# Optimization experiments

Measured on AMD Instinct MI355X. Metric: run time of the kernel, lower is better.

Reference implementation:

```python
import jax, jax.numpy as jnp
import numpy as np

N, D_IN, D_OUT, E, K = 32768, 1024, 1024, 8, 2
LN_EPS = 1e-5


def setup_inputs() -> dict:
    key = jax.random.key(0)
    ks = jax.random.split(key, 7)
    x = jax.random.normal(ks[0], (N, D_IN), dtype=jnp.float32)
    # gate: Linear(D_IN, E) then Tanh
    Wg = jax.random.normal(ks[1], (D_IN, E), dtype=jnp.float32) * 0.02
    bg = jnp.zeros((E,), dtype=jnp.float32)
    # experts: stacked Linear(D_IN, D_OUT) weights, [E, D_IN, D_OUT]
    We = jax.random.normal(ks[2], (E, D_IN, D_OUT), dtype=jnp.float32) * 0.02
    be = jnp.zeros((E, D_OUT), dtype=jnp.float32)
    # per-expert LayerNorm params
    gamma = jnp.ones((E, D_OUT), dtype=jnp.float32)
    beta = jnp.zeros((E, D_OUT), dtype=jnp.float32)
    return {"x": x, "Wg": Wg, "bg": bg, "We": We, "be": be,
            "gamma": gamma, "beta": beta}


def reference(x, Wg, bg, We, be, gamma, beta):
    # gating: Linear + Tanh, then top-k over experts, softmax over the k gates
    gate_logits = jnp.tanh(x @ Wg + bg)                      # [N, E]
    top_g, top_i = jax.lax.top_k(gate_logits, K)             # [N, K], [N, K]
    gates = jax.nn.softmax(top_g, axis=-1)                   # [N, K]

    # all experts computed densely (faithful to original): Linear + GELU + LN
    h = jnp.einsum('ni,eio->neo', x, We) + be[None]          # [N, E, D_OUT]
    h = jax.nn.gelu(h, approximate=False)                    # torch nn.GELU (exact)
    mu = jnp.mean(h, axis=-1, keepdims=True)
    var = jnp.mean(jnp.square(h - mu), axis=-1, keepdims=True)
    h = (h - mu) * jax.lax.rsqrt(var + LN_EPS)
    h = h * gamma[None] + beta[None]                         # [N, E, D_OUT]

    # gather top-k expert outputs and combine with softmax gates
    sel = jnp.take_along_axis(h, top_i[:, :, None], axis=1)  # [N, K, D_OUT]
    return jnp.sum(sel * gates[:, :, None], axis=1)          # [N, D_OUT]
```

## Files before the change

### kernel.cpp

```cpp
#include <hip/hip_runtime.h>
#include <hip/hip_bf16.h>

#define N_TOK 32768
#define D_IN 1024
#define D_OUT 1024
#define NE 8

#define BM 128
#define BN 128
#define BK 64
#define PAD 72

#define GBLK 64
#define GCH 64
#define NCH (D_IN / GCH)
#define CNT_STRIDE 64

typedef __attribute__((ext_vector_type(8))) short short8;
typedef __attribute__((ext_vector_type(4))) float floatx4;

__device__ __forceinline__ unsigned short f2bf(float f) {
    union { float f; unsigned u; } v; v.f = f;
    unsigned r = v.u + 0x7fffu + ((v.u >> 16) & 1u);
    return (unsigned short)(r >> 16);
}
__device__ __forceinline__ float bf2f(unsigned short u) {
    union { unsigned u; float f; } v; v.u = ((unsigned)u) << 16;
    return v.f;
}

__global__ void zero_cnt(int* __restrict__ cnt) {
    int i = blockIdx.x * 256 + threadIdx.x;
    if (i < 16 * CNT_STRIDE) cnt[i] = 0;
}

__global__ __launch_bounds__(256) void transpose_we(
    const float* __restrict__ We, unsigned short* __restrict__ WeT)
{
    __shared__ unsigned short tile[64 * 65];
    int e = blockIdx.z;
    int i0 = blockIdx.x * 64, o0 = blockIdx.y * 64;
    const float* src = We + ((size_t)e * D_IN + i0) * D_OUT + o0;
#pragma unroll
    for (int it = 0; it < 16; ++it) {
        int idx = threadIdx.x + it * 256;
        int r = idx >> 6, c = idx & 63;
        tile[r * 65 + c] = f2bf(src[(size_t)r * D_OUT + c]);
    }
    __syncthreads();
    unsigned short* dst = WeT + ((size_t)e * D_OUT + o0) * D_IN + i0;
#pragma unroll
    for (int it = 0; it < 16; ++it) {
        int idx = threadIdx.x + it * 256;
        int r = idx >> 6, c = idx & 63;
        dst[(size_t)r * D_IN + c] = tile[c * 65 + r];
    }
}

__global__ __launch_bounds__(256) void gate_kernel(
    const float* __restrict__ x, const float* __restrict__ Wg,
    const float* __restrict__ bg,
    int* __restrict__ top_i, float* __restrict__ gates,
    int* __restrict__ cnt, int* __restrict__ lists,
    unsigned short* __restrict__ xb)
{
    __shared__ float xs[GBLK][GCH + 1];
    __shared__ float wgs[4][136];
    __shared__ int lcnt[16];
    __shared__ int lbase[16];
    __shared__ int ltoks[16][GBLK];

    int tid = threadIdx.x;
    if (tid < 16) lcnt[tid] = 0;

    int tok0 = blockIdx.x * GBLK;
    int lane = tid & 63, wave = tid >> 6;
    int t = lane >> 2, q = lane & 3;
    int row = wave * 16 + t;
    int token = tok0 + row;

    double acc[NE] = {};

#pragma unroll 1
    for (int c = 0; c < NCH; ++c) {
        int cb = c * GCH;
        __syncthreads();
        {
            int i = tid;
#pragma unroll
            for (int it = 0; it < 2; ++it, i += 256) {
                float v = Wg[(size_t)cb * NE + i];
                int d = i >> 3, e = i & 7;
                wgs[d >> 4][(d & 15) * 8 + e] = v;
            }
        }
#pragma unroll
        for (int it = 0; it < 4; ++it) {
            int idx = tid + it * 256;
            int r = idx >> 4, c4 = (idx & 15) * 4;
            const float4 v = *(const float4*)(x + (size_t)(tok0 + r) * D_IN + cb + c4);
            xs[r][c4 + 0] = v.x; xs[r][c4 + 1] = v.y;
            xs[r][c4 + 2] = v.z; xs[r][c4 + 3] = v.w;
            ushort4 pk;
            pk.x = f2bf(v.x); pk.y = f2bf(v.y); pk.z = f2bf(v.z); pk.w = f2bf(v.w);
            *(ushort4*)(xb + (size_t)(tok0 + r) * D_IN + cb + c4) = pk;
        }
        __syncthreads();
#pragma unroll
        for (int jj = 0; jj < 16; ++jj) {
            double xd = (double)xs[row][q * 16 + jj];
            const float* wr = &wgs[q][jj * 8];
#pragma unroll
            for (int e = 0; e < NE; ++e)
                acc[e] += xd * (double)wr[e];
        }
    }

#pragma unroll
    for (int off = 1; off <= 2; off <<= 1)
#pragma unroll
        for (int e = 0; e < NE; ++e)
            acc[e] += __shfl_xor(acc[e], off, 64);

    float lg[NE];
#pragma unroll
    for (int e = 0; e < NE; ++e) lg[e] = tanhf((float)(acc[e] + (double)bg[e]));
    int i0 = 0;
    for (int e = 1; e < NE; ++e) if (lg[e] > lg[i0]) i0 = e;
    int i1 = (i0 == 0) ? 1 : 0;
    for (int e = 0; e < NE; ++e) { if (e == i0) continue; if (lg[e] > lg[i1]) i1 = e; }
    float tt = expf(lg[i1] - lg[i0]);
    float g0 = 1.0f / (1.0f + tt);
    float g1 = tt * g0;

    if (q == 0) {
        top_i[token * 2 + 0] = i0; top_i[token * 2 + 1] = i1;
        gates[token * 2 + 0] = g0; gates[token * 2 + 1] = g1;
        int p0 = atomicAdd(&lcnt[i0], 1);
        ltoks[i0][p0] = token;
        int p1 = atomicAdd(&lcnt[NE + i1], 1);
        ltoks[NE + i1][p1] = token;
    }
    __syncthreads();
    if (tid < 16) lbase[tid] = atomicAdd(&cnt[tid * CNT_STRIDE], lcnt[tid]);
    __syncthreads();
    int g = tid >> 4, j = tid & 15;
    int n = lcnt[g];
    int* dst = lists + (size_t)g * N_TOK + lbase[g];
    for (int k = j; k < n; k += 16) dst[k] = ltoks[g][k];
}

template <bool USEBF>
__global__ __launch_bounds__(256) void gemm_slot(
    const float* __restrict__ x, const unsigned short* __restrict__ xb,
    const unsigned short* __restrict__ WeT,
    const float* __restrict__ be, const int* __restrict__ lists,
    const int* __restrict__ cnt, int slot, unsigned short* __restrict__ h)
{
    int e = blockIdx.z;
    int count = cnt[(slot * NE + e) * CNT_STRIDE];
    int m0 = blockIdx.y * BM;
    if (m0 >= count) return;
    int n0 = blockIdx.x * BN;
    const int* list = lists + (size_t)(slot * NE + e) * N_TOK;

    __shared__ int toks[BM];
    __shared__ unsigned short As[BM * PAD];
    __shared__ unsigned short Bs[BN * PAD];

    int tid = threadIdx.x;
    if (tid < BM) {
        int r = m0 + tid; if (r > count - 1) r = count - 1;
        toks[tid] = list[r];
    }
    __syncthreads();

    int lane = tid & 63, wave = tid >> 6;
    int wm = (wave & 1) * 64, wn = (wave >> 1) * 64;
    int q = lane & 15, quad = lane >> 4;

    floatx4 acc[4][4] = {};

    const unsigned short* Bglob = WeT + ((size_t)e * D_OUT + n0) * D_IN;

    for (int kb = 0; kb < D_IN; kb += BK) {
        if (USEBF) {
#pragma unroll
            for (int it = 0; it < 4; ++it) {
                int idx = tid + it * 256;
                int m = idx >> 3, kq = idx & 7;
                *(uint4*)&As[m * PAD + kq * 8] =
                    *(const uint4*)(xb + (size_t)toks[m] * D_IN + kb + kq * 8);
            }
        } else {
#pragma unroll
            for (int it = 0; it < 8; ++it) {
                int idx = tid + it * 256;
                int m = idx >> 4, kq = idx & 15;
                float4 v = *(const float4*)(x + (size_t)toks[m] * D_IN + kb + kq * 4);
                ushort4 pk;
                pk.x = f2bf(v.x); pk.y = f2bf(v.y); pk.z = f2bf(v.z); pk.w = f2bf(v.w);
                *(ushort4*)&As[m * PAD + kq * 4] = pk;
            }
        }
#pragma unroll
        for (int it = 0; it < 4; ++it) {
            int idx = tid + it * 256;
            int n = idx >> 3, kq = idx & 7;
            *(uint4*)&Bs[n * PAD + kq * 8] =
                *(const uint4*)(Bglob + (size_t)n * D_IN + kb + kq * 8);
        }
        __syncthreads();

#pragma unroll
        for (int ks = 0; ks < BK; ks += 32) {
            short8 af[4], bfr[4];
#pragma unroll
            for (int i = 0; i < 4; ++i)
                af[i] = *(const short8*)&As[(wm + i * 16 + q) * PAD + ks + quad * 8];
#pragma unroll
            for (int j = 0; j < 4; ++j)
                bfr[j] = *(const short8*)&Bs[(wn + j * 16 + q) * PAD + ks + quad * 8];
#pragma unroll
            for (int i = 0; i < 4; ++i)
#pragma unroll
                for (int j = 0; j < 4; ++j)
                    acc[i][j] = __builtin_amdgcn_mfma_f32_16x16x32_bf16(
                        af[i], bfr[j], acc[i][j], 0, 0, 0);
        }
        __syncthreads();
    }

#pragma unroll
    for (int i = 0; i < 4; ++i) {
#pragma unroll
        for (int r = 0; r < 4; ++r) {
            int m = wm + i * 16 + quad * 4 + r;
            if (m0 + m < count) {
                int tok = toks[m];
#pragma unroll
                for (int j = 0; j < 4; ++j) {
                    int n = n0 + wn + j * 16 + q;
                    float v = acc[i][j][r] + be[(size_t)e * D_OUT + n];
                    h[(size_t)tok * D_OUT + n] = f2bf(v);
                }
            }
        }
    }
}

__global__ __launch_bounds__(256) void ln_combine(
    const unsigned short* __restrict__ h, const float* __restrict__ gamma,
    const float* __restrict__ beta, const float* __restrict__ gates,
    const int* __restrict__ top_i, int slot, float* __restrict__ out)
{
    int wave = threadIdx.x >> 6, lane = threadIdx.x & 63;
    int token = blockIdx.x * 4 + wave;
    int e = top_i[token * 2 + slot];
    float gate = gates[token * 2 + slot];
    const unsigned short* hr = h + (size_t)token * D_OUT;

    float g[16], sum = 0.f, sumsq = 0.f;
#pragma unroll
    for (int jj = 0; jj < 4; ++jj) {
        int n = jj * 256 + lane * 4;
        uint2 pk = *(const uint2*)(hr + n);
        float v0 = bf2f((unsigned short)(pk.x & 0xffff));
        float v1 = bf2f((unsigned short)(pk.x >> 16));
        float v2 = bf2f((unsigned short)(pk.y & 0xffff));
        float v3 = bf2f((unsigned short)(pk.y >> 16));
        float g0 = 0.5f * v0 * (1.0f + erff(v0 * 0.70710678118654752f));
        float g1 = 0.5f * v1 * (1.0f + erff(v1 * 0.70710678118654752f));
        float g2 = 0.5f * v2 * (1.0f + erff(v2 * 0.70710678118654752f));
        float g3 = 0.5f * v3 * (1.0f + erff(v3 * 0.70710678118654752f));
        g[jj * 4 + 0] = g0; g[jj * 4 + 1] = g1; g[jj * 4 + 2] = g2; g[jj * 4 + 3] = g3;
        sum   += g0 + g1 + g2 + g3;
        sumsq += g0 * g0 + g1 * g1 + g2 * g2 + g3 * g3;
    }
#pragma unroll
    for (int off = 32; off; off >>= 1) {
        sum   += __shfl_xor(sum, off, 64);
        sumsq += __shfl_xor(sumsq, off, 64);
    }
    float mu  = sum * (1.0f / 1024.0f);
    float var = sumsq * (1.0f / 1024.0f) - mu * mu;
    float rs  = rsqrtf(var + 1e-5f);

    const float* gm = gamma + (size_t)e * D_OUT;
    const float* bt = beta  + (size_t)e * D_OUT;
    float* orow = out + (size_t)token * D_OUT;
#pragma unroll
    for (int jj = 0; jj < 4; ++jj) {
        int n = jj * 256 + lane * 4;
        float4 gm4 = *(const float4*)(gm + n);
        float4 bt4 = *(const float4*)(bt + n);
        float4 o;
        o.x = gate * ((g[jj * 4 + 0] - mu) * rs * gm4.x + bt4.x);
        o.y = gate * ((g[jj * 4 + 1] - mu) * rs * gm4.y + bt4.y);
        o.z = gate * ((g[jj * 4 + 2] - mu) * rs * gm4.z + bt4.z);
        o.w = gate * ((g[jj * 4 + 3] - mu) * rs * gm4.w + bt4.w);
        if (slot == 0) {
            *(float4*)(orow + n) = o;
        } else {
            float4 p = *(const float4*)(orow + n);
            p.x += o.x; p.y += o.y; p.z += o.z; p.w += o.w;
            *(float4*)(orow + n) = p;
        }
    }
}

extern "C" void kernel_launch(void* const* d_in, const int* in_sizes, int n_in,
                              void* d_out, int out_size, void* d_ws, size_t ws_size,
                              hipStream_t stream) {
    const float* x     = (const float*)d_in[0];
    const float* Wg    = (const float*)d_in[1];
    const float* bg    = (const float*)d_in[2];
    const float* We    = (const float*)d_in[3];
    const float* be    = (const float*)d_in[4];
    const float* gamma = (const float*)d_in[5];
    const float* beta  = (const float*)d_in[6];
    float* out = (float*)d_out;

    char* w = (char*)d_ws;
    size_t off = 0;
    int*   cnt   = (int*)(w + off);            off += (size_t)16 * CNT_STRIDE * 4;
    int*   top_i = (int*)(w + off);            off += (size_t)N_TOK * 2 * 4;
    float* gates = (float*)(w + off);          off += (size_t)N_TOK * 2 * 4;
    int*   lists = (int*)(w + off);            off += (size_t)16 * N_TOK * 4;
    unsigned short* WeT = (unsigned short*)(w + off); off += (size_t)NE * D_IN * D_OUT * 2;
    unsigned short* h   = (unsigned short*)(w + off); off += (size_t)N_TOK * D_OUT * 2;
    size_t xb_bytes = (size_t)N_TOK * D_IN * 2;
    bool use_bf = (off + xb_bytes) <= ws_size;
    unsigned short* xb = use_bf ? (unsigned short*)(w + off) : h;
    if (use_bf) off += xb_bytes;

    zero_cnt<<<(16 * CNT_STRIDE + 255) / 256, 256, 0, stream>>>(cnt);
    transpose_we<<<dim3(16, 16, NE), 256, 0, stream>>>(We, WeT);
    gate_kernel<<<N_TOK / GBLK, 256, 0, stream>>>(x, Wg, bg, top_i, gates, cnt, lists, xb);
    for (int s = 0; s < 2; ++s) {
        if (use_bf)
            gemm_slot<true><<<dim3(D_OUT / BN, N_TOK / BM, NE), 256, 0, stream>>>(
                x, xb, WeT, be, lists, cnt, s, h);
        else
            gemm_slot<false><<<dim3(D_OUT / BN, N_TOK / BM, NE), 256, 0, stream>>>(
                x, xb, WeT, be, lists, cnt, s, h);
        ln_combine<<<N_TOK / 4, 256, 0, stream>>>(h, gamma, beta, gates, top_i, s, out);
    }
}
```

Before: 644.4 us.

## Use direct global-to-LDS loads with XOR swizzle and fuse both slots

The bf16 GEMM now loads A and B tiles straight into LDS with global_load_lds, using an XOR-swizzled unpadded layout in place of the register-staged padded copy. When workspace allows, both top-k slots run in a single GEMM launch that writes two separate h buffers, and a new combine kernel normalises both expert outputs and writes the output once instead of doing a read-modify-write. The aim is to cut VGPR staging and load latency, drop kernel launches, and halve traffic on the output. It needs an extra N×D_OUT bf16 workspace buffer, and the swizzle and LDS-destination indexing must line up with the per-wave write pattern of the direct loads.

```diff
diff --git a/kernel.cpp b/kernel.cpp
--- a/kernel.cpp
+++ b/kernel.cpp
@@ -16,6 +16,9 @@
 #define NCH (D_IN / GCH)
 #define CNT_STRIDE 64
 
+#define AS1 __attribute__((address_space(1)))
+#define AS3 __attribute__((address_space(3)))
+
 typedef __attribute__((ext_vector_type(8))) short short8;
 typedef __attribute__((ext_vector_type(4))) float floatx4;
 
@@ -27,6 +30,11 @@
 __device__ __forceinline__ float bf2f(unsigned short u) {
     union { unsigned u; float f; } v; v.u = ((unsigned)u) << 16;
     return v.f;
+}
+
+__device__ __forceinline__ void gl_lds16(const void* g, void* l) {
+    __builtin_amdgcn_global_load_lds((const AS1 unsigned int*)g,
+                                     (AS3 unsigned int*)l, 16, 0, 0);
 }
 
 __global__ void zero_cnt(int* __restrict__ cnt) {
@@ -150,9 +158,113 @@
     for (int k = j; k < n; k += 16) dst[k] = ltoks[g][k];
 }
 
-template <bool USEBF>
-__global__ __launch_bounds__(256) void gemm_slot(
-    const float* __restrict__ x, const unsigned short* __restrict__ xb,
+__global__ __launch_bounds__(256) void gemm_slot2(
+    const unsigned short* __restrict__ xb,
+    const unsigned short* __restrict__ WeT,
+    const float* __restrict__ be, const int* __restrict__ lists,
+    const int* __restrict__ cnt, int zoff,
+    unsigned short* __restrict__ h0, unsigned short* __restrict__ h1)
+{
+    int z = blockIdx.z + zoff;
+    int slot = z >> 3, e = z & 7;
+    unsigned short* __restrict__ h = slot ? h1 : h0;
+    int count = cnt[z * CNT_STRIDE];
+    int m0 = blockIdx.y * BM;
+    if (m0 >= count) return;
+    int n0 = blockIdx.x * BN;
+    const int* list = lists + (size_t)z * N_TOK;
+
+    __shared__ int toks[BM];
+    __shared__ __align__(16) unsigned short As[BM * BK];
+    __shared__ __align__(16) unsigned short Bs[BN * BK];
+
+    int tid = threadIdx.x;
+    if (tid < BM) {
+        int r = m0 + tid; if (r > count - 1) r = count - 1;
+        toks[tid] = list[r];
+    }
+    __syncthreads();
+
+    int lane = tid & 63, wave = tid >> 6;
+    int wm = (wave & 1) * 64, wn = (wave >> 1) * 64;
+    int q = lane & 15, quad = lane >> 4;
+
+    const unsigned short* Bglob = WeT + ((size_t)e * D_OUT + n0) * D_IN;
+
+    const unsigned short* asrc[4];
+    const unsigned short* bsrc[4];
+    unsigned short* adst[4];
+    unsigned short* bdst[4];
+#pragma unroll
+    for (int it = 0; it < 4; ++it) {
+        int idx = tid + it * 256;
+        int m = idx >> 3, c = idx & 7;
+        int sc = c ^ (m & 7);
+        asrc[it] = xb + (size_t)toks[m] * D_IN + sc * 8;
+        bsrc[it] = Bglob + (size_t)m * D_IN + sc * 8;
+        unsigned short* base = (unsigned short*)0;
+        adst[it] = As + (size_t)(it * 256 + (tid & 192)) * 8;
+        bdst[it] = Bs + (size_t)(it * 256 + (tid & 192)) * 8;
+        (void)base;
+    }
+
+    floatx4 acc[4][4] = {};
+
+    for (int kb = 0; kb < D_IN; kb += BK) {
+#pragma unroll
+        for (int it = 0; it < 4; ++it)
+            gl_lds16(asrc[it] + kb, adst[it]);
+#pragma unroll
+        for (int it = 0; it < 4; ++it)
+            gl_lds16(bsrc[it] + kb, bdst[it]);
+        __syncthreads();
+
+#pragma unroll
+        for (int ks = 0; ks < BK; ks += 32) {
+            int cb = ks >> 3;
+            short8 af[4], bfr[4];
+#pragma unroll
+            for (int i = 0; i < 4; ++i) {
+                int row = wm + i * 16 + q;
+                int ch = (cb + quad) ^ (row & 7);
+                af[i] = *(const short8*)&As[row * BK + ch * 8];
+            }
+#pragma unroll
+            for (int j = 0; j < 4; ++j) {
+                int row = wn + j * 16 + q;
+                int ch = (cb + quad) ^ (row & 7);
+                bfr[j] = *(const short8*)&Bs[row * BK + ch * 8];
+            }
+#pragma unroll
+            for (int i = 0; i < 4; ++i)
+#pragma unroll
+                for (int j = 0; j < 4; ++j)
+                    acc[i][j] = __builtin_amdgcn_mfma_f32_16x16x32_bf16(
+                        af[i], bfr[j], acc[i][j], 0, 0, 0);
+        }
+        __syncthreads();
+    }
+
+#pragma unroll
+    for (int i = 0; i < 4; ++i) {
+#pragma unroll
+        for (int r = 0; r < 4; ++r) {
+            int m = wm + i * 16 + quad * 4 + r;
+            if (m0 + m < count) {
+                int tok = toks[m];
+#pragma unroll
+                for (int j = 0; j < 4; ++j) {
+                    int n = n0 + wn + j * 16 + q;
+                    float v = acc[i][j][r] + be[(size_t)e * D_OUT + n];
+                    h[(size_t)tok * D_OUT + n] = f2bf(v);
+                }
+            }
+        }
+    }
+}
+
+__global__ __launch_bounds__(256) void gemm_slot_f32(
+    const float* __restrict__ x,
     const unsigned short* __restrict__ WeT,
     const float* __restrict__ be, const int* __restrict__ lists,
     const int* __restrict__ cnt, int slot, unsigned short* __restrict__ h)
@@ -180,28 +292,17 @@
     int q = lane & 15, quad = lane >> 4;
 
     floatx4 acc[4][4] = {};
-
     const unsigned short* Bglob = WeT + ((size_t)e * D_OUT + n0) * D_IN;
 
     for (int kb = 0; kb < D_IN; kb += BK) {
-        if (USEBF) {
-#pragma unroll
-            for (int it = 0; it < 4; ++it) {
-                int idx = tid + it * 256;
-                int m = idx >> 3, kq = idx & 7;
-                *(uint4*)&As[m * PAD + kq * 8] =
-                    *(const uint4*)(xb + (size_t)toks[m] * D_IN + kb + kq * 8);
-            }
-        } else {
-#pragma unroll
-            for (int it = 0; it < 8; ++it) {
-                int idx = tid + it * 256;
-                int m = idx >> 4, kq = idx & 15;
-                float4 v = *(const float4*)(x + (size_t)toks[m] * D_IN + kb + kq * 4);
-                ushort4 pk;
-                pk.x = f2bf(v.x); pk.y = f2bf(v.y); pk.z = f2bf(v.z); pk.w = f2bf(v.w);
-                *(ushort4*)&As[m * PAD + kq * 4] = pk;
-            }
+#pragma unroll
+        for (int it = 0; it < 8; ++it) {
+            int idx = tid + it * 256;
+            int m = idx >> 4, kq = idx & 15;
+            float4 v = *(const float4*)(x + (size_t)toks[m] * D_IN + kb + kq * 4);
+            ushort4 pk;
+            pk.x = f2bf(v.x); pk.y = f2bf(v.y); pk.z = f2bf(v.z); pk.w = f2bf(v.w);
+            *(ushort4*)&As[m * PAD + kq * 4] = pk;
         }
 #pragma unroll
         for (int it = 0; it < 4; ++it) {
@@ -211,7 +312,6 @@
                 *(const uint4*)(Bglob + (size_t)n * D_IN + kb + kq * 8);
         }
         __syncthreads();
-
 #pragma unroll
         for (int ks = 0; ks < BK; ks += 32) {
             short8 af[4], bfr[4];
@@ -309,6 +409,76 @@
     }
 }
 
+__global__ __launch_bounds__(256) void ln_combine2(
+    const unsigned short* __restrict__ h0, const unsigned short* __restrict__ h1,
+    const float* __restrict__ gamma, const float* __restrict__ beta,
+    const float* __restrict__ gates, const int* __restrict__ top_i,
+    float* __restrict__ out)
+{
+    int wave = threadIdx.x >> 6, lane = threadIdx.x & 63;
+    int token = blockIdx.x * 4 + wave;
+    int e0 = top_i[token * 2 + 0], e1 = top_i[token * 2 + 1];
+    float gate0 = gates[token * 2 + 0], gate1 = gates[token * 2 + 1];
+
+    float g[2][16], mu[2], rs[2];
+    const unsigned short* hr[2] = { h0 + (size_t)token * D_OUT,
+                                    h1 + (size_t)token * D_OUT };
+#pragma unroll
+    for (int s = 0; s < 2; ++s) {
+        float sum = 0.f, sumsq = 0.f;
+#pragma unroll
+        for (int jj = 0; jj < 4; ++jj) {
+            int n = jj * 256 + lane * 4;
+            uint2 pk = *(const uint2*)(hr[s] + n);
+            float v0 = bf2f((unsigned short)(pk.x & 0xffff));
+            float v1 = bf2f((unsigned short)(pk.x >> 16));
+            float v2 = bf2f((unsigned short)(pk.y & 0xffff));
+            float v3 = bf2f((unsigned short)(pk.y >> 16));
+            float a0 = 0.5f * v0 * (1.0f + erff(v0 * 0.70710678118654752f));
+            float a1 = 0.5f * v1 * (1.0f + erff(v1 * 0.70710678118654752f));
+            float a2 = 0.5f * v2 * (1.0f + erff(v2 * 0.70710678118654752f));
+            float a3 = 0.5f * v3 * (1.0f + erff(v3 * 0.70710678118654752f));
+            g[s][jj * 4 + 0] = a0; g[s][jj * 4 + 1] = a1;
+            g[s][jj * 4 + 2] = a2; g[s][jj * 4 + 3] = a3;
+            sum   += a0 + a1 + a2 + a3;
+            sumsq += a0 * a0 + a1 * a1 + a2 * a2 + a3 * a3;
+        }
+#pragma unroll
+        for (int off = 32; off; off >>= 1) {
+            sum   += __shfl_xor(sum, off, 64);
+            sumsq += __shfl_xor(sumsq, off, 64);
+        }
+        float m = sum * (1.0f / 1024.0f);
+        float var = sumsq * (1.0f / 1024.0f) - m * m;
+        mu[s] = m;
+        rs[s] = rsqrtf(var + 1e-5f);
+    }
+
+    const float* gm0 = gamma + (size_t)e0 * D_OUT;
+    const float* bt0 = beta  + (size_t)e0 * D_OUT;
+    const float* gm1 = gamma + (size_t)e1 * D_OUT;
+    const float* bt1 = beta  + (size_t)e1 * D_OUT;
+    float* orow = out + (size_t)token * D_OUT;
+#pragma unroll
+    for (int jj = 0; jj < 4; ++jj) {
+        int n = jj * 256 + lane * 4;
+        float4 gmA = *(const float4*)(gm0 + n);
+        float4 btA = *(const float4*)(bt0 + n);
+        float4 gmB = *(const float4*)(gm1 + n);
+        float4 btB = *(const float4*)(bt1 + n);
+        float4 o;
+        o.x = gate0 * ((g[0][jj * 4 + 0] - mu[0]) * rs[0] * gmA.x + btA.x)
+            + gate1 * ((g[1][jj * 4 + 0] - mu[1]) * rs[1] * gmB.x + btB.x);
+        o.y = gate0 * ((g[0][jj * 4 + 1] - mu[0]) * rs[0] * gmA.y + btA.y)
+            + gate1 * ((g[1][jj * 4 + 1] - mu[1]) * rs[1] * gmB.y + btB.y);
+        o.z = gate0 * ((g[0][jj * 4 + 2] - mu[0]) * rs[0] * gmA.z + btA.z)
+            + gate1 * ((g[1][jj * 4 + 2] - mu[1]) * rs[1] * gmB.z + btB.z);
+        o.w = gate0 * ((g[0][jj * 4 + 3] - mu[0]) * rs[0] * gmA.w + btA.w)
+            + gate1 * ((g[1][jj * 4 + 3] - mu[1]) * rs[1] * gmB.w + btB.w);
+        *(float4*)(orow + n) = o;
+    }
+}
+
 extern "C" void kernel_launch(void* const* d_in, const int* in_sizes, int n_in,
                               void* d_out, int out_size, void* d_ws, size_t ws_size,
                               hipStream_t stream) {
@@ -333,17 +503,30 @@
     bool use_bf = (off + xb_bytes) <= ws_size;
     unsigned short* xb = use_bf ? (unsigned short*)(w + off) : h;
     if (use_bf) off += xb_bytes;
+    size_t h1_bytes = (size_t)N_TOK * D_OUT * 2;
+    bool use_fused = use_bf && (off + h1_bytes) <= ws_size;
+    unsigned short* h1 = use_fused ? (unsigned short*)(w + off) : h;
+    if (use_fused) off += h1_bytes;
 
     zero_cnt<<<(16 * CNT_STRIDE + 255) / 256, 256, 0, stream>>>(cnt);
     transpose_we<<<dim3(16, 16, NE), 256, 0, stream>>>(We, WeT);
     gate_kernel<<<N_TOK / GBLK, 256, 0, stream>>>(x, Wg, bg, top_i, gates, cnt, lists, xb);
-    for (int s = 0; s < 2; ++s) {
-        if (use_bf)
-            gemm_slot<true><<<dim3(D_OUT / BN, N_TOK / BM, NE), 256, 0, stream>>>(
-                x, xb, WeT, be, lists, cnt, s, h);
-        else
-            gemm_slot<false><<<dim3(D_OUT / BN, N_TOK / BM, NE), 256, 0, stream>>>(
-                x, xb, WeT, be, lists, cnt, s, h);
-        ln_combine<<<N_TOK / 4, 256, 0, stream>>>(h, gamma, beta, gates, top_i, s, out);
-    }
-}
+
+    if (use_fused) {
+        gemm_slot2<<<dim3(D_OUT / BN, N_TOK / BM, 16), 256, 0, stream>>>(
+            xb, WeT, be, lists, cnt, 0, h, h1);
+        ln_combine2<<<N_TOK / 4, 256, 0, stream>>>(h, h1, gamma, beta, gates, top_i, out);
+    } else if (use_bf) {
+        for (int s = 0; s < 2; ++s) {
+            gemm_slot2<<<dim3(D_OUT / BN, N_TOK / BM, 8), 256, 0, stream>>>(
+                xb, WeT, be, lists, cnt, s * 8, h, h);
+            ln_combine<<<N_TOK / 4, 256, 0, stream>>>(h, gamma, beta, gates, top_i, s, out);
+        }
+    } else {
+        for (int s = 0; s < 2; ++s) {
+            gemm_slot_f32<<<dim3(D_OUT / BN, N_TOK / BM, 8), 256, 0, stream>>>(
+                x, WeT, be, lists, cnt, s, h);
+            ln_combine<<<N_TOK / 4, 256, 0, stream>>>(h, gamma, beta, gates, top_i, s, out);
+        }
+    }
+}
```

New measurement: 583.0 us. -9.5%, faster.
